# Optimization experiments

Measured on AMD Instinct MI355X. Metric: run time of the kernel, lower is better.

## Reference

```python
import jax, jax.numpy as jnp
import numpy as np
from jax.ops import segment_sum, segment_max

N_NODES = 100000
N_EDGES = 1600000


def _glorot(key, shape):
    fan_in, fan_out = shape[0], shape[-1]
    lim = np.sqrt(6.0 / (fan_in + fan_out))
    return jax.random.uniform(key, shape, jnp.float32, -lim, lim)


def setup_inputs() -> dict:
    key = jax.random.key(0)
    ks = jax.random.split(key, 12)
    x = jax.random.normal(ks[0], (N_NODES, 7), jnp.float32)
    edge_index = jax.random.randint(ks[1], (2, N_EDGES), 0, N_NODES, jnp.int64)
    return {
        "x": x,
        "edge_index": edge_index,
        # GCNConv(7, 32)
        "W1": _glorot(ks[2], (7, 32)), "b1": jnp.zeros((32,), jnp.float32),
        # GATConv(32, 64), heads=1
        "W2": _glorot(ks[3], (32, 64)), "a_src2": _glorot(ks[4], (64, 1))[:, 0],
        "a_dst2": _glorot(ks[5], (64, 1))[:, 0], "b2": jnp.zeros((64,), jnp.float32),
        # GCNConv(64, 128)
        "W3": _glorot(ks[6], (64, 128)), "b3": jnp.zeros((128,), jnp.float32),
        # GATConv(128, 2), heads=1
        "W4": _glorot(ks[7], (128, 2)), "a_src4": _glorot(ks[8], (2, 1))[:, 0],
        "a_dst4": _glorot(ks[9], (2, 1))[:, 0], "b4": jnp.zeros((2,), jnp.float32),
    }


def _gcn_conv(x, src, dst, W, b):
    # x' = W x; symmetric normalization with self-loops already in (src, dst)
    h = x @ W
    deg = segment_sum(jnp.ones_like(dst, dtype=h.dtype), dst, num_segments=N_NODES)
    dinv = jnp.where(deg > 0, jax.lax.rsqrt(deg), 0.0)
    norm = dinv[src] * dinv[dst]            # [E]
    msg = norm[:, None] * h[src]            # [E, C]
    return segment_sum(msg, dst, num_segments=N_NODES) + b


def _gat_conv(x, src, dst, W, a_src, a_dst, b, slope=0.2):
    h = x @ W                               # [N, C]
    alpha_src = h @ a_src                   # [N]
    alpha_dst = h @ a_dst                   # [N]
    e = alpha_src[src] + alpha_dst[dst]     # [E]
    e = jnp.where(e > 0, e, slope * e)      # leaky_relu
    # numerically-stable softmax over edges grouped by destination node
    m = segment_max(e, dst, num_segments=N_NODES)
    ex = jnp.exp(e - m[dst])
    denom = segment_sum(ex, dst, num_segments=N_NODES)
    w = ex / (denom[dst] + 1e-16)           # [E]
    out = segment_sum(w[:, None] * h[src], dst, num_segments=N_NODES)
    return out + b


def reference(x, edge_index, W1, b1, W2, a_src2, a_dst2, b2, W3, b3, W4, a_src4, a_dst4, b4):
    # add self-loops once (PyG does it per layer; identical edge set each time)
    loop = jnp.arange(N_NODES, dtype=edge_index.dtype)
    src = jnp.concatenate([edge_index[0], loop])
    dst = jnp.concatenate([edge_index[1], loop])

    h = _gcn_conv(x, src, dst, W1, b1)
    h = jax.nn.relu(h)
    h = _gat_conv(h, src, dst, W2, a_src2, a_dst2, b2)
    h = jax.nn.relu(h)
    h = _gcn_conv(h, src, dst, W3, b3)
    h = jax.nn.relu(h)
    h = _gat_conv(h, src, dst, W4, a_src4, a_dst4, b4)
    return jax.nn.log_softmax(h, axis=1)
```

## Files before the change

kernel.cpp:

```cpp
#include <hip/hip_runtime.h>
#include <hip/hip_bf16.h>

#define NN 100000
#define NE 1600000
#define NT (NN + NE)
#define NBKT 256
#define BSZ 391
#define BCAP 10240

typedef unsigned int u32;
typedef unsigned short u16;

static __device__ __forceinline__ int clampN(int s) {
    return ((unsigned)s < (unsigned)NN) ? s : 0;
}
static __device__ __forceinline__ int ld_src(const int* ei, int is32, int e) {
    return is32 ? ei[e] : ei[2 * e];
}
static __device__ __forceinline__ int ld_dst(const int* ei, int is32, int e) {
    return is32 ? ei[NE + e] : ei[2 * NE + 2 * e];
}
static __device__ __forceinline__ float2 b2x2(u32 u) {
    float2 r;
    r.x = __uint_as_float((u & 0xffffu) << 16);
    r.y = __uint_as_float(u & 0xffff0000u);
    return r;
}
static __device__ __forceinline__ u16 f2bs(float f) {
    union { __hip_bfloat16 b; u16 u; } cv;
    cv.b = __float2bfloat16(f);
    return cv.u;
}
static __device__ __forceinline__ u32 pack2(float x, float y) {
    return ((u32)f2bs(y) << 16) | (u32)f2bs(x);
}
static __device__ __forceinline__ float lrelu_c(float e) {
    e = (e > 0.f) ? e : 0.2f * e;
    return fminf(e, 60.f);
}

#define FMA4(acc, s, v) { acc.x += (s)*(v).x; acc.y += (s)*(v).y; \
                          acc.z += (s)*(v).z; acc.w += (s)*(v).w; }


__global__ void __launch_bounds__(256) k_init(const float* __restrict__ W2,
                                              const float* __restrict__ a2s,
                                              const float* __restrict__ a2d,
                                              const int* __restrict__ ei,
                                              float* __restrict__ va2,
                                              float* __restrict__ vd2,
                                              int* __restrict__ flag,
                                              int* __restrict__ gcur) {
    if (blockIdx.x == 0) {
        if (threadIdx.x == 0) flag[0] = 0;
        __syncthreads();
        int nz = 0;
        for (int i = threadIdx.x; i < 4096; i += 256) nz |= ei[2 * i + 1];
        if (nz) atomicOr(flag, 1);
        if (threadIdx.x < NBKT) gcur[threadIdx.x] = 0;
    } else if (threadIdx.x < 64) {
        int t = threadIdx.x;
        if (t < 32) {
            float a = 0.f;
            for (int c = 0; c < 64; c++) a += W2[t * 64 + c] * a2s[c];
            va2[t] = a;
        } else {
            int k = t - 32;
            float a = 0.f;
            for (int c = 0; c < 64; c++) a += W2[k * 64 + c] * a2d[c];
            vd2[k] = a;
        }
    }
}


__global__ void __launch_bounds__(256) k_binA(const int* __restrict__ ei,
                                              const int* __restrict__ flag,
                                              int* __restrict__ gcur,
                                              u32* __restrict__ staging) {
    __shared__ int hist[NBKT];
    __shared__ int gbase[NBKT];
    __shared__ int cnt2[NBKT];
    int tid = threadIdx.x;
    if (tid < NBKT) hist[tid] = 0;
    __syncthreads();

    int base = blockIdx.x * 4096;
    int is32 = flag[0];
    int d[16], s[16];
    #pragma unroll
    for (int i = 0; i < 16; i++) {
        int e = base + i * 256 + tid;
        d[i] = -1;
        if (e < NE) {
            int dd = ld_dst(ei, is32, e);
            if ((unsigned)dd < (unsigned)NN) { d[i] = dd; s[i] = clampN(ld_src(ei, is32, e)); }
        } else if (e < NT) {
            d[i] = e - NE; s[i] = e - NE;
        }
        if (d[i] >= 0) atomicAdd(&hist[d[i] / BSZ], 1);
    }
    __syncthreads();
    if (tid < NBKT) {
        int c = hist[tid];
        gbase[tid] = c ? atomicAdd(&gcur[tid], c) : 0;
        cnt2[tid] = 0;
    }
    __syncthreads();
    #pragma unroll
    for (int i = 0; i < 16; i++) {
        if (d[i] >= 0) {
            int b = d[i] / BSZ;
            int pos = gbase[b] + atomicAdd(&cnt2[b], 1);
            if (pos < BCAP)
                staging[(size_t)b * BCAP + pos] =
                    ((unsigned)(d[i] - b * BSZ) << 17) | (unsigned)s[i];
        }
    }
}

__global__ void __launch_bounds__(256) k_histscan(const u32* __restrict__ staging,
                                                  const int* __restrict__ gcur,
                                                  const float* __restrict__ x,
                                                  u32* __restrict__ xpb,
                                                  int* __restrict__ rowptr,
                                                  int* __restrict__ deg,
                                                  int* __restrict__ part) {
    __shared__ int h[512];
    __shared__ int sm[256];
    int b = blockIdx.x, tid = threadIdx.x;
    h[tid] = 0; h[tid + 256] = 0;
    __syncthreads();
    int cnt = min(gcur[b], BCAP);
    const u32* st = staging + (size_t)b * BCAP;
    for (int i = tid; i < cnt; i += 256)
        atomicAdd(&h[st[i] >> 17], 1);
    __syncthreads();
    int h0 = h[2 * tid], h1 = h[2 * tid + 1];
    int pair = h0 + h1;
    sm[tid] = pair;
    __syncthreads();
    for (int off = 1; off < 256; off <<= 1) {
        int t = (tid >= off) ? sm[tid - off] : 0;
        __syncthreads();
        sm[tid] += t;
        __syncthreads();
    }
    int excl = sm[tid] - pair;
    int g0 = b * BSZ + 2 * tid;
    if (2 * tid < BSZ && g0 < NN) { rowptr[g0] = excl; deg[g0] = h0; }
    int g1 = g0 + 1;
    if (2 * tid + 1 < BSZ && g1 < NN) { rowptr[g1] = excl + h0; deg[g1] = h1; }
    if (tid == 255) part[b] = sm[255];

    for (int i = b * 256 + tid; i < NN * 4; i += NBKT * 256) {
        int n = i >> 2, c2 = i & 3;
        float f0 = x[n * 7 + 2 * c2];
        float f1 = (2 * c2 + 1 < 7) ? x[n * 7 + 2 * c2 + 1] : 0.f;
        xpb[i] = pack2(f0, f1);
    }
}

__global__ void __launch_bounds__(256) k_scat(const u32* __restrict__ staging,
                                              const int* __restrict__ gcur,
                                              const int* __restrict__ part,
                                              int* __restrict__ rowptr,
                                              const int* __restrict__ deg,
                                              float* __restrict__ dinv,
                                              int* __restrict__ col) {
    __shared__ int sm[256];
    __shared__ int cur[BSZ];
    int b = blockIdx.x, tid = threadIdx.x;
    int v = part[tid];
    sm[tid] = v;
    __syncthreads();
    for (int off = 1; off < 256; off <<= 1) {
        int t = (tid >= off) ? sm[tid - off] : 0;
        __syncthreads();
        sm[tid] += t;
        __syncthreads();
    }
    int pb = (b > 0) ? sm[b - 1] : 0;
    if (b == 0 && tid == 0) rowptr[NN] = NT;
    for (int l = tid; l < BSZ; l += 256) {
        int g = b * BSZ + l;
        if (g < NN) {
            int r = rowptr[g] + pb;
            rowptr[g] = r;
            cur[l] = r;
            int d = deg[g];
            dinv[g] = rsqrtf((float)(d > 0 ? d : 1));
        } else cur[l] = 0;
    }
    __syncthreads();
    int cnt = min(gcur[b], BCAP);
    const u32* st = staging + (size_t)b * BCAP;
    for (int i = tid; i < cnt; i += 256) {
        u32 w = st[i];
        int l = w >> 17;
        int s = w & 0x1FFFF;
        int p = atomicAdd(&cur[l], 1);
        if ((unsigned)p < (unsigned)NT) col[p] = s;
    }
}


__global__ void __launch_bounds__(256) k_l1(const u32* __restrict__ xpb,
                                            const int* __restrict__ rowptr,
                                            const int* __restrict__ col,
                                            const float* __restrict__ dinv,
                                            const float* __restrict__ W1,
                                            const float* __restrict__ b1,
                                            const float* __restrict__ va2,
                                            const float* __restrict__ vd2,
                                            u32* __restrict__ O1b,
                                            float* __restrict__ as_,
                                            float* __restrict__ ad_) {
    __shared__ float sW1[7 * 32];
    __shared__ float sb1[32], sva[32], svd[32];
    __shared__ float sT1[64 * 8];
    if (threadIdx.x < 224) sW1[threadIdx.x] = W1[threadIdx.x];
    else {
        int c = threadIdx.x - 224;
        sb1[c] = b1[c]; sva[c] = va2[c]; svd[c] = vd2[c];
    }
    int node_l = threadIdx.x >> 2;
    int lane = threadIdx.x & 3;
    int n = blockIdx.x * 64 + node_l;
    if (n < NN) {
        int beg = rowptr[n], end = rowptr[n + 1];
        float ax = 0.f, ay = 0.f;
        #pragma unroll 4
        for (int e = beg; e < end; e++) {
            int s = clampN(col[e]);
            float w = dinv[s];
            float2 f = b2x2(xpb[(size_t)s * 4 + lane]);
            ax += w * f.x;
            ay += w * f.y;
        }
        float dn = dinv[n];
        sT1[node_l * 8 + lane * 2] = ax * dn;
        sT1[node_l * 8 + lane * 2 + 1] = ay * dn;
    }
    __syncthreads();
    if (n >= NN) return;
    int c8 = lane * 8;
    float4 aA = {0,0,0,0}, aB = {0,0,0,0};
    #pragma unroll
    for (int k = 0; k < 7; k++) {
        float t = sT1[node_l * 8 + k];
        float4 wva = *(const float4*)&sW1[k * 32 + c8];
        float4 wvb = *(const float4*)&sW1[k * 32 + c8 + 4];
        FMA4(aA, t, wva);
        FMA4(aB, t, wvb);
    }
    float o0 = fmaxf(aA.x + sb1[c8], 0.f);
    float o1 = fmaxf(aA.y + sb1[c8 + 1], 0.f);
    float o2 = fmaxf(aA.z + sb1[c8 + 2], 0.f);
    float o3 = fmaxf(aA.w + sb1[c8 + 3], 0.f);
    float o4 = fmaxf(aB.x + sb1[c8 + 4], 0.f);
    float o5 = fmaxf(aB.y + sb1[c8 + 5], 0.f);
    float o6 = fmaxf(aB.z + sb1[c8 + 6], 0.f);
    float o7 = fmaxf(aB.w + sb1[c8 + 7], 0.f);
    uint4 pk = {pack2(o0, o1), pack2(o2, o3), pack2(o4, o5), pack2(o6, o7)};
    *(uint4*)(O1b + (size_t)n * 16 + lane * 4) = pk;
    float vs = o0 * sva[c8] + o1 * sva[c8 + 1] + o2 * sva[c8 + 2] + o3 * sva[c8 + 3]
             + o4 * sva[c8 + 4] + o5 * sva[c8 + 5] + o6 * sva[c8 + 6] + o7 * sva[c8 + 7];
    float vd = o0 * svd[c8] + o1 * svd[c8 + 1] + o2 * svd[c8 + 2] + o3 * svd[c8 + 3]
             + o4 * svd[c8 + 4] + o5 * svd[c8 + 5] + o6 * svd[c8 + 6] + o7 * svd[c8 + 7];
    vs += __shfl_xor(vs, 1, 4); vs += __shfl_xor(vs, 2, 4);
    vd += __shfl_xor(vd, 1, 4); vd += __shfl_xor(vd, 2, 4);
    if (lane == 0) { as_[n] = vs; ad_[n] = vd; }
}


__global__ void __launch_bounds__(256) k_l2(const u32* __restrict__ O1b,
                                            const float* __restrict__ as_,
                                            const float* __restrict__ ad_,
                                            const int* __restrict__ rowptr,
                                            const int* __restrict__ col,
                                            const float* __restrict__ W2,
                                            const float* __restrict__ b2,
                                            const float* __restrict__ dinv,
                                            u32* __restrict__ O2b) {
    __shared__ float sW2[32 * 64];
    __shared__ float sT2[32 * 36];
    __shared__ float sb2[64];
    {
        const float4* g = (const float4*)W2;
        float4* s4 = (float4*)sW2;
        s4[threadIdx.x] = g[threadIdx.x];
        s4[threadIdx.x + 256] = g[threadIdx.x + 256];
    }
    if (threadIdx.x < 64) sb2[threadIdx.x] = b2[threadIdx.x];

    int node_l = threadIdx.x >> 3;
    int lane = threadIdx.x & 7;
    int n = blockIdx.x * 32 + node_l;
    {
        int beg = rowptr[n], end = rowptr[n + 1];
        float adn = ad_[n];
        float den = 0.f;
        float4 acc = {0, 0, 0, 0};
        #pragma unroll 2
        for (int e = beg; e < end; e++) {
            int s = clampN(col[e]);
            float p = __expf(lrelu_c(as_[s] + adn));
            den += p;
            uint2 w = *(const uint2*)(O1b + (size_t)s * 16 + lane * 2);
            float2 f0 = b2x2(w.x), f1 = b2x2(w.y);
            acc.x += p * f0.x; acc.y += p * f0.y; acc.z += p * f1.x; acc.w += p * f1.y;
        }
        float inv = 1.0f / (den + 1e-16f);
        acc.x *= inv; acc.y *= inv; acc.z *= inv; acc.w *= inv;
        *(float4*)&sT2[node_l * 36 + lane * 4] = acc;
    }
    __syncthreads();

    int grp = threadIdx.x >> 4;
    int l = threadIdx.x & 15;
    int c4 = l * 4;
    int lbase = grp * 2;

    float4 acc0 = {0,0,0,0}, acc1 = {0,0,0,0};
    #pragma unroll
    for (int k4 = 0; k4 < 8; k4++) {
        float4 t0 = *(const float4*)&sT2[(lbase + 0) * 36 + 4 * k4];
        float4 t1 = *(const float4*)&sT2[(lbase + 1) * 36 + 4 * k4];
        #pragma unroll
        for (int j = 0; j < 4; j++) {
            float4 wv = *(const float4*)&sW2[(4 * k4 + j) * 64 + c4];
            FMA4(acc0, ((const float*)&t0)[j], wv);
            FMA4(acc1, ((const float*)&t1)[j], wv);
        }
    }
    float4 bb = *(const float4*)&sb2[c4];
    int n0 = blockIdx.x * 32 + lbase;
    float d0 = dinv[n0], d1 = dinv[n0 + 1];
    {
        float o0 = fmaxf(acc0.x + bb.x, 0.f) * d0;
        float o1 = fmaxf(acc0.y + bb.y, 0.f) * d0;
        float o2 = fmaxf(acc0.z + bb.z, 0.f) * d0;
        float o3 = fmaxf(acc0.w + bb.w, 0.f) * d0;
        uint2 pk = {pack2(o0, o1), pack2(o2, o3)};
        *(uint2*)(O2b + (size_t)n0 * 32 + l * 2) = pk;
    }
    {
        float o0 = fmaxf(acc1.x + bb.x, 0.f) * d1;
        float o1 = fmaxf(acc1.y + bb.y, 0.f) * d1;
        float o2 = fmaxf(acc1.z + bb.z, 0.f) * d1;
        float o3 = fmaxf(acc1.w + bb.w, 0.f) * d1;
        uint2 pk = {pack2(o0, o1), pack2(o2, o3)};
        *(uint2*)(O2b + (size_t)(n0 + 1) * 32 + l * 2) = pk;
    }
}


__global__ void __launch_bounds__(512) k_l3(const u32* __restrict__ O2b,
                                            const int* __restrict__ rowptr,
                                            const int* __restrict__ col,
                                            const float* __restrict__ dinv,
                                            const float* __restrict__ W3,
                                            const float* __restrict__ b3,
                                            const float* __restrict__ W4,
                                            const float* __restrict__ av4s,
                                            const float* __restrict__ av4d,
                                            float4* __restrict__ h4as,
                                            float* __restrict__ ad_) {
    __shared__ float sW3[64 * 128];
    __shared__ float sT3[64 * 64];
    __shared__ float sW4[128 * 2];
    __shared__ float sb3[128];

    float4 wreg[4];
    {
        const float4* g = (const float4*)W3;
        #pragma unroll
        for (int i = 0; i < 4; i++) wreg[i] = g[threadIdx.x + 512 * i];
    }
    if (threadIdx.x < 128) {
        sb3[threadIdx.x] = b3[threadIdx.x];
        sW4[2 * threadIdx.x] = W4[2 * threadIdx.x];
        sW4[2 * threadIdx.x + 1] = W4[2 * threadIdx.x + 1];
    }

    int node_l = threadIdx.x >> 3;
    int lane = threadIdx.x & 7;
    int n = blockIdx.x * 64 + node_l;
    if (n < NN) {
        int beg = rowptr[n], end = rowptr[n + 1];
        float4 accA = {0,0,0,0}, accB = {0,0,0,0};
        #pragma unroll 4
        for (int e = beg; e < end; e++) {
            int s = clampN(col[e]);
            uint4 w = *(const uint4*)(O2b + (size_t)s * 32 + lane * 4);
            float2 f0 = b2x2(w.x), f1 = b2x2(w.y), f2 = b2x2(w.z), f3 = b2x2(w.w);
            accA.x += f0.x; accA.y += f0.y; accA.z += f1.x; accA.w += f1.y;
            accB.x += f2.x; accB.y += f2.y; accB.z += f3.x; accB.w += f3.y;
        }
        float dn = dinv[n];
        accA.x *= dn; accA.y *= dn; accA.z *= dn; accA.w *= dn;
        accB.x *= dn; accB.y *= dn; accB.z *= dn; accB.w *= dn;
        float* dst = &sT3[node_l * 64 + lane * 8];
        *(float4*)dst = accA;
        *(float4*)(dst + 4) = accB;
    }
    {
        float4* s4 = (float4*)sW3;
        #pragma unroll
        for (int i = 0; i < 4; i++) s4[threadIdx.x + 512 * i] = wreg[i];
    }
    __syncthreads();

    int w = threadIdx.x >> 6;
    int lane64 = threadIdx.x & 63;
    int half = lane64 >> 5;
    int lw = lane64 & 31;
    int lbase = w * 8 + half * 4;
    int c4 = lw * 4;

    float4 acc0 = {0,0,0,0}, acc1 = {0,0,0,0}, acc2 = {0,0,0,0}, acc3 = {0,0,0,0};
    #pragma unroll 4
    for (int k4 = 0; k4 < 16; k4++) {
        float4 t0 = *(const float4*)&sT3[(lbase + 0) * 64 + 4 * k4];
        float4 t1 = *(const float4*)&sT3[(lbase + 1) * 64 + 4 * k4];
        float4 t2 = *(const float4*)&sT3[(lbase + 2) * 64 + 4 * k4];
        float4 t3 = *(const float4*)&sT3[(lbase + 3) * 64 + 4 * k4];
        #pragma unroll
        for (int j = 0; j < 4; j++) {
            float4 wv = *(const float4*)&sW3[(4 * k4 + j) * 128 + c4];
            FMA4(acc0, ((const float*)&t0)[j], wv);
            FMA4(acc1, ((const float*)&t1)[j], wv);
            FMA4(acc2, ((const float*)&t2)[j], wv);
            FMA4(acc3, ((const float*)&t3)[j], wv);
        }
    }

    float4 bb = *(const float4*)&sb3[c4];
    float w40x = sW4[2 * c4],     w41x = sW4[2 * c4 + 1];
    float w40y = sW4[2 * c4 + 2], w41y = sW4[2 * c4 + 3];
    float w40z = sW4[2 * c4 + 4], w41z = sW4[2 * c4 + 5];
    float w40w = sW4[2 * c4 + 6], w41w = sW4[2 * c4 + 7];
    float av4s0 = av4s[0], av4s1 = av4s[1];
    float av4d0 = av4d[0], av4d1 = av4d[1];

    #pragma unroll
    for (int ni = 0; ni < 4; ni++) {
        float4 a = (ni == 0) ? acc0 : (ni == 1) ? acc1 : (ni == 2) ? acc2 : acc3;
        a.x = fmaxf(a.x + bb.x, 0.f);
        a.y = fmaxf(a.y + bb.y, 0.f);
        a.z = fmaxf(a.z + bb.z, 0.f);
        a.w = fmaxf(a.w + bb.w, 0.f);
        float p0 = a.x * w40x + a.y * w40y + a.z * w40z + a.w * w40w;
        float p1 = a.x * w41x + a.y * w41y + a.z * w41z + a.w * w41w;
        #pragma unroll
        for (int off = 16; off > 0; off >>= 1) {
            p0 += __shfl_down(p0, off, 32);
            p1 += __shfl_down(p1, off, 32);
        }
        if (lw == 0) {
            int gn = blockIdx.x * 64 + lbase + ni;
            if (gn < NN) {
                float asv = p0 * av4s0 + p1 * av4s1;
                float4 pk = {p0, p1, asv, 0.f};
                h4as[gn] = pk;
                ad_[gn] = p0 * av4d0 + p1 * av4d1;
            }
        }
    }
}


__global__ void k_final(const float4* __restrict__ h4as,
                        const float* __restrict__ ad_, const int* __restrict__ rowptr,
                        const int* __restrict__ col, const float* __restrict__ b,
                        float* __restrict__ out) {
    int gid = blockIdx.x * 256 + threadIdx.x;
    int n = gid >> 2;
    if (n >= NN) return;
    int lsub = gid & 3;
    int beg = rowptr[n], end = rowptr[n + 1];
    float adn = ad_[n];
    float den = 0.f, a0 = 0.f, a1 = 0.f;
    for (int e = beg + lsub; e < end; e += 4) {
        int s = clampN(col[e]);
        float4 h = h4as[s];
        float p = __expf(lrelu_c(h.z + adn));
        den += p;
        a0 += p * h.x;
        a1 += p * h.y;
    }
    den += __shfl_xor(den, 1, 4); den += __shfl_xor(den, 2, 4);
    a0  += __shfl_xor(a0, 1, 4);  a0  += __shfl_xor(a0, 2, 4);
    a1  += __shfl_xor(a1, 1, 4);  a1  += __shfl_xor(a1, 2, 4);
    if (lsub == 0) {
        float inv = 1.0f / (den + 1e-16f);
        float v0 = a0 * inv + b[0];
        float v1 = a1 * inv + b[1];
        float mx = fmaxf(v0, v1);
        float lse = mx + logf(__expf(v0 - mx) + __expf(v1 - mx));
        float2 o = {v0 - lse, v1 - lse};
        *(float2*)(out + n * 2) = o;
    }
}

__global__ void k_sentinel(float* __restrict__ out, float v) {
    int i = blockIdx.x * 256 + threadIdx.x;
    if (i < NN * 2) out[i] = v;
}


extern "C" void kernel_launch(void* const* d_in, const int* in_sizes, int n_in,
                              void* d_out, int out_size, void* d_ws, size_t ws_size,
                              hipStream_t stream) {
    const float* x    = (const float*)d_in[0];
    const int* ei     = (const int*)d_in[1];
    const float* W1   = (const float*)d_in[2];
    const float* b1   = (const float*)d_in[3];
    const float* W2   = (const float*)d_in[4];
    const float* a2s  = (const float*)d_in[5];
    const float* a2d  = (const float*)d_in[6];
    const float* b2   = (const float*)d_in[7];
    const float* W3   = (const float*)d_in[8];
    const float* b3   = (const float*)d_in[9];
    const float* W4   = (const float*)d_in[10];
    const float* a4s  = (const float*)d_in[11];
    const float* a4d  = (const float*)d_in[12];
    const float* b4   = (const float*)d_in[13];
    float* out = (float*)d_out;

    char* base = (char*)d_ws;
    size_t off = 0;
    auto alloc = [&](size_t bytes) {
        char* q = base + off;
        off += (bytes + 255) & ~(size_t)255;
        return q;
    };
    u32* xpb     = (u32*)alloc((size_t)NN * 4 * 4);
    u32* O1b     = (u32*)alloc((size_t)NN * 16 * 4);
    u32* O2b     = (u32*)alloc((size_t)NN * 32 * 4);
    u32* staging = (u32*)alloc((size_t)NBKT * BCAP * 4);
    int* col     = (int*)alloc((size_t)NT * 4);
    int* rowptr  = (int*)alloc((size_t)(NN + 1) * 4);
    int* deg     = (int*)alloc((size_t)NN * 4);
    float* dinv  = (float*)alloc((size_t)NN * 4);
    float* as_   = (float*)alloc((size_t)NN * 4);
    float* ad_   = (float*)alloc((size_t)NN * 4);
    float4* h4as = (float4*)alloc((size_t)NN * 16);
    int* part    = (int*)alloc(512 * 4);
    int* flag    = (int*)alloc(256);
    int* gcur    = (int*)alloc(NBKT * 4);
    float* va2   = (float*)alloc(32 * 4);
    float* vd2   = (float*)alloc(32 * 4);

    float code = 0.f;
    if (off > ws_size)            code = 1000.f + (float)(ws_size >> 20);
    else if (n_in != 14)          code = 2000.f + 10.f * (float)n_in;
    else if (out_size != NN * 2)  code = 3400.f;
    if (code != 0.f) {
        k_sentinel<<<(NN * 2 + 255) / 256, 256, 0, stream>>>(out, code);
        return;
    }

    const int NTILE = (NT + 4095) / 4096;

    k_init<<<2, 256, 0, stream>>>(W2, a2s, a2d, ei, va2, vd2, flag, gcur);
    k_binA<<<NTILE, 256, 0, stream>>>(ei, flag, gcur, staging);
    k_histscan<<<NBKT, 256, 0, stream>>>(staging, gcur, x, xpb, rowptr, deg, part);
    k_scat<<<NBKT, 256, 0, stream>>>(staging, gcur, part, rowptr, deg, dinv, col);

    k_l1<<<(NN + 63) / 64, 256, 0, stream>>>(xpb, rowptr, col, dinv,
                                             W1, b1, va2, vd2, O1b, as_, ad_);
    k_l2<<<NN / 32, 256, 0, stream>>>(O1b, as_, ad_, rowptr, col,
                                      W2, b2, dinv, O2b);
    k_l3<<<(NN + 63) / 64, 512, 0, stream>>>(O2b, rowptr, col, dinv,
                                             W3, b3, W4, a4s, a4d, h4as, ad_);
    k_final<<<NN * 4 / 256 + 1, 256, 0, stream>>>(h4as, ad_, rowptr, col, b4, out);
}
```

Baseline: 258.0 us.

## Replace block barriers with wave barriers by keeping node rows wave-local

```diff
diff --git a/kernel.cpp b/kernel.cpp
--- a/kernel.cpp
+++ b/kernel.cpp
@@ -224,10 +224,13 @@
         int c = threadIdx.x - 224;
         sb1[c] = b1[c]; sva[c] = va2[c]; svd[c] = vd2[c];
     }
+    __syncthreads();
+
     int node_l = threadIdx.x >> 2;
     int lane = threadIdx.x & 3;
     int n = blockIdx.x * 64 + node_l;
-    if (n < NN) {
+    if (n >= NN) return;
+    {
         int beg = rowptr[n], end = rowptr[n + 1];
         float ax = 0.f, ay = 0.f;
         #pragma unroll 4
@@ -242,8 +245,7 @@
         sT1[node_l * 8 + lane * 2] = ax * dn;
         sT1[node_l * 8 + lane * 2 + 1] = ay * dn;
     }
-    __syncthreads();
-    if (n >= NN) return;
+    __builtin_amdgcn_wave_barrier();
     int c8 = lane * 8;
     float4 aA = {0,0,0,0}, aB = {0,0,0,0};
     #pragma unroll
@@ -293,6 +295,7 @@
         s4[threadIdx.x + 256] = g[threadIdx.x + 256];
     }
     if (threadIdx.x < 64) sb2[threadIdx.x] = b2[threadIdx.x];
+    __syncthreads();
 
     int node_l = threadIdx.x >> 3;
     int lane = threadIdx.x & 7;
@@ -315,7 +318,7 @@
         acc.x *= inv; acc.y *= inv; acc.z *= inv; acc.w *= inv;
         *(float4*)&sT2[node_l * 36 + lane * 4] = acc;
     }
-    __syncthreads();
+    __builtin_amdgcn_wave_barrier();
 
     int grp = threadIdx.x >> 4;
     int l = threadIdx.x & 15;
@@ -368,105 +371,95 @@
                                             float4* __restrict__ h4as,
                                             float* __restrict__ ad_) {
     __shared__ float sW3[64 * 128];
-    __shared__ float sT3[64 * 64];
+    __shared__ float sT3[64 * 68];
     __shared__ float sW4[128 * 2];
     __shared__ float sb3[128];
 
-    float4 wreg[4];
     {
         const float4* g = (const float4*)W3;
+        float4* s4 = (float4*)sW3;
         #pragma unroll
-        for (int i = 0; i < 4; i++) wreg[i] = g[threadIdx.x + 512 * i];
+        for (int i = 0; i < 4; i++) s4[threadIdx.x + 512 * i] = g[threadIdx.x + 512 * i];
     }
     if (threadIdx.x < 128) {
         sb3[threadIdx.x] = b3[threadIdx.x];
         sW4[2 * threadIdx.x] = W4[2 * threadIdx.x];
         sW4[2 * threadIdx.x + 1] = W4[2 * threadIdx.x + 1];
     }
-
-    int node_l = threadIdx.x >> 3;
-    int lane = threadIdx.x & 7;
-    int n = blockIdx.x * 64 + node_l;
-    if (n < NN) {
+    __syncthreads();
+
+    int w = threadIdx.x >> 6;
+    int l = threadIdx.x & 63;
+    int node_sub = l >> 3;
+    int cl = l & 7;
+    int row = w * 8 + node_sub;
+    int n = blockIdx.x * 64 + row;
+    if (n >= NN) return;
+
+    {
         int beg = rowptr[n], end = rowptr[n + 1];
         float4 accA = {0,0,0,0}, accB = {0,0,0,0};
         #pragma unroll 4
         for (int e = beg; e < end; e++) {
             int s = clampN(col[e]);
-            uint4 w = *(const uint4*)(O2b + (size_t)s * 32 + lane * 4);
-            float2 f0 = b2x2(w.x), f1 = b2x2(w.y), f2 = b2x2(w.z), f3 = b2x2(w.w);
+            uint4 wd = *(const uint4*)(O2b + (size_t)s * 32 + cl * 4);
+            float2 f0 = b2x2(wd.x), f1 = b2x2(wd.y), f2 = b2x2(wd.z), f3 = b2x2(wd.w);
             accA.x += f0.x; accA.y += f0.y; accA.z += f1.x; accA.w += f1.y;
             accB.x += f2.x; accB.y += f2.y; accB.z += f3.x; accB.w += f3.y;
         }
         float dn = dinv[n];
         accA.x *= dn; accA.y *= dn; accA.z *= dn; accA.w *= dn;
         accB.x *= dn; accB.y *= dn; accB.z *= dn; accB.w *= dn;
-        float* dst = &sT3[node_l * 64 + lane * 8];
+        float* dst = &sT3[row * 68 + cl * 8];
         *(float4*)dst = accA;
         *(float4*)(dst + 4) = accB;
     }
-    {
-        float4* s4 = (float4*)sW3;
-        #pragma unroll
-        for (int i = 0; i < 4; i++) s4[threadIdx.x + 512 * i] = wreg[i];
-    }
-    __syncthreads();
-
-    int w = threadIdx.x >> 6;
-    int lane64 = threadIdx.x & 63;
-    int half = lane64 >> 5;
-    int lw = lane64 & 31;
-    int lbase = w * 8 + half * 4;
-    int c4 = lw * 4;
-
+    __builtin_amdgcn_wave_barrier();
+
+    const float* trow = &sT3[row * 68];
     float4 acc0 = {0,0,0,0}, acc1 = {0,0,0,0}, acc2 = {0,0,0,0}, acc3 = {0,0,0,0};
     #pragma unroll 4
     for (int k4 = 0; k4 < 16; k4++) {
-        float4 t0 = *(const float4*)&sT3[(lbase + 0) * 64 + 4 * k4];
-        float4 t1 = *(const float4*)&sT3[(lbase + 1) * 64 + 4 * k4];
-        float4 t2 = *(const float4*)&sT3[(lbase + 2) * 64 + 4 * k4];
-        float4 t3 = *(const float4*)&sT3[(lbase + 3) * 64 + 4 * k4];
+        float4 t4 = *(const float4*)&trow[k4 * 4];
         #pragma unroll
         for (int j = 0; j < 4; j++) {
-            float4 wv = *(const float4*)&sW3[(4 * k4 + j) * 128 + c4];
-            FMA4(acc0, ((const float*)&t0)[j], wv);
-            FMA4(acc1, ((const float*)&t1)[j], wv);
-            FMA4(acc2, ((const float*)&t2)[j], wv);
-            FMA4(acc3, ((const float*)&t3)[j], wv);
-        }
-    }
-
-    float4 bb = *(const float4*)&sb3[c4];
-    float w40x = sW4[2 * c4],     w41x = sW4[2 * c4 + 1];
-    float w40y = sW4[2 * c4 + 2], w41y = sW4[2 * c4 + 3];
-    float w40z = sW4[2 * c4 + 4], w41z = sW4[2 * c4 + 5];
-    float w40w = sW4[2 * c4 + 6], w41w = sW4[2 * c4 + 7];
+            float tj = ((const float*)&t4)[j];
+            const float* wr = &sW3[(k4 * 4 + j) * 128 + 4 * cl];
+            float4 w0 = *(const float4*)&wr[0];
+            float4 w1 = *(const float4*)&wr[32];
+            float4 w2 = *(const float4*)&wr[64];
+            float4 w3v = *(const float4*)&wr[96];
+            FMA4(acc0, tj, w0);
+            FMA4(acc1, tj, w1);
+            FMA4(acc2, tj, w2);
+            FMA4(acc3, tj, w3v);
+        }
+    }
+
     float av4s0 = av4s[0], av4s1 = av4s[1];
     float av4d0 = av4d[0], av4d1 = av4d[1];
-
+    float p0 = 0.f, p1 = 0.f;
     #pragma unroll
-    for (int ni = 0; ni < 4; ni++) {
-        float4 a = (ni == 0) ? acc0 : (ni == 1) ? acc1 : (ni == 2) ? acc2 : acc3;
+    for (int q = 0; q < 4; q++) {
+        float4 a = (q == 0) ? acc0 : (q == 1) ? acc1 : (q == 2) ? acc2 : acc3;
+        int c = 4 * cl + 32 * q;
+        float4 bb = *(const float4*)&sb3[c];
         a.x = fmaxf(a.x + bb.x, 0.f);
         a.y = fmaxf(a.y + bb.y, 0.f);
         a.z = fmaxf(a.z + bb.z, 0.f);
         a.w = fmaxf(a.w + bb.w, 0.f);
-        float p0 = a.x * w40x + a.y * w40y + a.z * w40z + a.w * w40w;
-        float p1 = a.x * w41x + a.y * w41y + a.z * w41z + a.w * w41w;
-        #pragma unroll
-        for (int off = 16; off > 0; off >>= 1) {
-            p0 += __shfl_down(p0, off, 32);
-            p1 += __shfl_down(p1, off, 32);
-        }
-        if (lw == 0) {
-            int gn = blockIdx.x * 64 + lbase + ni;
-            if (gn < NN) {
-                float asv = p0 * av4s0 + p1 * av4s1;
-                float4 pk = {p0, p1, asv, 0.f};
-                h4as[gn] = pk;
-                ad_[gn] = p0 * av4d0 + p1 * av4d1;
-            }
-        }
+        p0 += a.x * sW4[2 * c]     + a.y * sW4[2 * (c + 1)]
+            + a.z * sW4[2 * (c + 2)] + a.w * sW4[2 * (c + 3)];
+        p1 += a.x * sW4[2 * c + 1]     + a.y * sW4[2 * (c + 1) + 1]
+            + a.z * sW4[2 * (c + 2) + 1] + a.w * sW4[2 * (c + 3) + 1];
+    }
+    p0 += __shfl_xor(p0, 1, 8); p0 += __shfl_xor(p0, 2, 8); p0 += __shfl_xor(p0, 4, 8);
+    p1 += __shfl_xor(p1, 1, 8); p1 += __shfl_xor(p1, 2, 8); p1 += __shfl_xor(p1, 4, 8);
+    if (cl == 0) {
+        float asv = p0 * av4s0 + p1 * av4s1;
+        float4 pk = {p0, p1, asv, 0.f};
+        h4as[n] = pk;
+        ad_[n] = p0 * av4d0 + p1 * av4d1;
     }
 }
 
```

Result: no change. 253.8 us (-1.6%).
